# Performance work log

Measured on AMD Instinct MI355X. Metric: run time of the kernel, lower is better.

Reference implementation:

```python
import jax, jax.numpy as jnp
import numpy as np

N = 8            # n_qubits
N_LAYERS_CRZ = 1

_H = jnp.array([[1.0, 1.0], [1.0, -1.0]], dtype=jnp.complex64) / np.sqrt(2).astype(np.float32)
_X2 = jnp.array([[0.0, 1.0], [1.0, 0.0]], dtype=jnp.complex64)
_I2 = jnp.eye(2, dtype=jnp.complex64)


def _apply_1q(state, U, q):
    # shared (2,2) gate on wire q; state: (B, 2,...,2)
    moved = jnp.moveaxis(state, 1 + q, -1)
    out = jnp.einsum('ij,...j->...i', U, moved)
    return jnp.moveaxis(out, -1, 1 + q)


def _apply_1q_batched(state, U, q):
    # per-sample (B,2,2) gate on wire q
    moved = jnp.moveaxis(state, 1 + q, -1)
    out = jnp.einsum('bij,b...j->b...i', U, moved)
    return jnp.moveaxis(out, -1, 1 + q)


def _apply_diag_batched(state, d, q):
    # per-sample diagonal (B,2) phases on wire q
    shape = (d.shape[0],) + (1,) * q + (2,) + (1,) * (N - 1 - q)
    return state * d.reshape(shape)


def _apply_ctrl_diag(state, ph, c, t):
    # controlled diagonal: apply phases ph (2,) on target t when control c == 1
    moved = jnp.moveaxis(state, (1 + c, 1 + t), (-2, -1))
    d = jnp.stack([jnp.ones(2, state.dtype), ph])  # (bc, bt)
    moved = moved * d
    return jnp.moveaxis(moved, (-2, -1), (1 + c, 1 + t))


def _apply_ctrl(state, U, c, t):
    # controlled (2,2) gate, control c, target t
    moved = jnp.moveaxis(state, (1 + c, 1 + t), (-2, -1))
    s0 = moved[..., 0, :]
    s1 = jnp.einsum('ij,...j->...i', U, moved[..., 1, :])
    out = jnp.stack([s0, s1], axis=-2)
    return jnp.moveaxis(out, (-2, -1), (1 + c, 1 + t))


def _circuit(X, weights):
    B = X.shape[0]
    state = jnp.zeros((B,) + (2,) * N, jnp.complex64)
    state = state.at[(slice(None),) + (0,) * N].set(1.0)

    # encoding: H, RZ(x[2q]), RY(x[2q+1]) on each wire q (2q+1 < 16 always)
    for q in range(N):
        state = _apply_1q(state, _H, q)
        th_z = X[:, 2 * q]
        d = jnp.stack([jnp.exp(-0.5j * th_z), jnp.exp(0.5j * th_z)], axis=-1)  # (B,2)
        state = _apply_diag_batched(state, d, q)
        half = 0.5 * X[:, 2 * q + 1]
        c, s = jnp.cos(half), jnp.sin(half)
        Ury = jnp.stack([jnp.stack([c, -s], -1), jnp.stack([s, c], -1)], -2)  # (B,2,2) real
        state = _apply_1q_batched(state, Ury, q)

    # CRZ ring
    for l in range(N_LAYERS_CRZ):
        for i in range(N):
            th = weights[l, i]
            ph = jnp.stack([jnp.exp(-0.5j * th), jnp.exp(0.5j * th)])
            state = _apply_ctrl_diag(state, ph, i, (i + 1) % N)

    # all-to-all CRX
    for i in range(N):
        for j in range(N):
            if j == i:
                continue
            half = 0.5 * weights[N_LAYERS_CRZ + i, j]
            Urx = jnp.cos(half) * _I2 + (-1j * jnp.sin(half)) * _X2
            state = _apply_ctrl(state, Urx, i, j)

    probs = jnp.real(state * jnp.conj(state)).reshape(B, 2 ** N)
    q_idx = jnp.arange(N)
    bits = (jnp.arange(2 ** N)[None, :] >> (N - 1 - q_idx)[:, None]) & 1  # (N, 2^N)
    signs = (1.0 - 2.0 * bits).astype(probs.dtype)
    return probs @ signs.T  # (B, N) <Z_q> expectations


def setup_inputs() -> dict:
    key = jax.random.key(0)
    k1, k2 = jax.random.split(key)
    X = jax.random.normal(k1, (16384, 2 * N), dtype=jnp.float32)
    weights = jax.random.normal(k2, (N_LAYERS_CRZ + N, (N_LAYERS_CRZ + N) * N), dtype=jnp.float32)
    return {"X": X, "weights": weights}


def reference(X, weights):
    return _circuit(X, weights)
```

## Files before the change

kernel.cpp:

```cpp
#include <hip/hip_runtime.h>


static __device__ __forceinline__ float rlane(float v, int src) {
    return __int_as_float(__builtin_amdgcn_readlane(__float_as_int(v), src));
}
template <int CTRL>
static __device__ __forceinline__ float dppf(float x) {
    return __int_as_float(__builtin_amdgcn_update_dpp(0, __float_as_int(x), CTRL, 0xF, 0xF, true));
}
static __device__ __forceinline__ float xor1f(float x) { return dppf<0xB1>(x); }
static __device__ __forceinline__ float xor2f(float x) { return dppf<0x4E>(x); }
static __device__ __forceinline__ float xor4f(float x) { return dppf<0x1B>(dppf<0x141>(x)); }
static __device__ __forceinline__ float xor8f(float x) { return dppf<0x128>(x); }

__global__ __launch_bounds__(256, 4) void qsim_kernel(const float* __restrict__ X,
                                                      const float* __restrict__ W,
                                                      float* __restrict__ out,
                                                      int B) {
    const int lane = threadIdx.x & 63;
    const int g = lane >> 4;
    const int s = lane & 15;
    const int b = (blockIdx.x * 4 + (threadIdx.x >> 6)) * 4 + g;
    const bool active = (b < B);
    const int bc = active ? b : (B - 1);

    float gcv = 1.0f, gsv = 0.0f;
    if (lane < 56) {
        const int i = lane / 7;
        const int jj = lane - 7 * i;
        const int j = jj + (jj >= i ? 1 : 0);
        const float h = 0.5f * W[(1 + i) * 72 + j];
        __sincosf(h, &gsv, &gcv);
    }

    float u0r, u0i, u1r, u1i;
    {
        const int q = s & 7;
        float2 xq = ((const float2*)X)[bc * 8 + q];
        float cz, sz, cy, sy;
        __sincosf(0.5f * xq.x, &sz, &cz);
        __sincosf(0.5f * xq.y, &sy, &cy);
        u0r = (cy - sy) * cz;  u0i = -(cy + sy) * sz;
        u1r = (cy + sy) * cz;  u1i = (cy - sy) * sz;
    }

    float Pr = 1.0f, Pi = 0.0f;
#pragma unroll
    for (int q = 0; q < 4; ++q) {
        const int src = (g << 4) + q;
        const float a0r = __shfl(u0r, src, 64), a0i = __shfl(u0i, src, 64);
        const float a1r = __shfl(u1r, src, 64), a1i = __shfl(u1i, src, 64);
        const int bit = (s >> (3 - q)) & 1;
        const float vr = bit ? a1r : a0r;
        const float vi = bit ? a1i : a0i;
        const float nr = Pr * vr - Pi * vi;
        const float ni = Pr * vi + Pi * vr;
        Pr = nr; Pi = ni;
    }
    float w0r[4], w0i[4], w1r[4], w1i[4];
#pragma unroll
    for (int q = 4; q < 8; ++q) {
        const int src = (g << 4) + q;
        w0r[q - 4] = __shfl(u0r, src, 64);  w0i[q - 4] = __shfl(u0i, src, 64);
        w1r[q - 4] = __shfl(u1r, src, 64);  w1i[q - 4] = __shfl(u1i, src, 64);
    }
    float ar[16], ai[16];
    {
        float t1r[2], t1i[2];
        t1r[0] = w0r[0]; t1i[0] = w0i[0];
        t1r[1] = w1r[0]; t1i[1] = w1i[0];
        float t2r[4], t2i[4];
#pragma unroll
        for (int h = 0; h < 2; ++h) {
            t2r[h * 2 + 0] = t1r[h] * w0r[1] - t1i[h] * w0i[1];
            t2i[h * 2 + 0] = t1r[h] * w0i[1] + t1i[h] * w0r[1];
            t2r[h * 2 + 1] = t1r[h] * w1r[1] - t1i[h] * w1i[1];
            t2i[h * 2 + 1] = t1r[h] * w1i[1] + t1i[h] * w1r[1];
        }
        float t3r[8], t3i[8];
#pragma unroll
        for (int h = 0; h < 4; ++h) {
            t3r[h * 2 + 0] = t2r[h] * w0r[2] - t2i[h] * w0i[2];
            t3i[h * 2 + 0] = t2r[h] * w0i[2] + t2i[h] * w0r[2];
            t3r[h * 2 + 1] = t2r[h] * w1r[2] - t2i[h] * w1i[2];
            t3i[h * 2 + 1] = t2r[h] * w1i[2] + t2i[h] * w1r[2];
        }
#pragma unroll
        for (int h = 0; h < 8; ++h) {
            const float m0r = t3r[h] * w0r[3] - t3i[h] * w0i[3];
            const float m0i = t3r[h] * w0i[3] + t3i[h] * w0r[3];
            const float m1r = t3r[h] * w1r[3] - t3i[h] * w1i[3];
            const float m1i = t3r[h] * w1i[3] + t3i[h] * w1r[3];
            ar[h * 2 + 0] = Pr * m0r - Pi * m0i;
            ai[h * 2 + 0] = Pr * m0i + Pi * m0r;
            ar[h * 2 + 1] = Pr * m1r - Pi * m1i;
            ai[h * 2 + 1] = Pr * m1i + Pi * m1r;
        }
    }

    {
        const float w0 = W[0], w1 = W[1], w2 = W[2], w3 = W[3];
        const float w4 = W[4], w5 = W[5], w6 = W[6], w7 = W[7];
        const int b7 = (s >> 3) & 1, b6 = (s >> 2) & 1, b5 = (s >> 1) & 1, b4 = s & 1;
        float phiS = 0.0f;
        phiS += b7 ? (b6 ? w0 : -w0) : 0.0f;
        phiS += b6 ? (b5 ? w1 : -w1) : 0.0f;
        phiS += b5 ? (b4 ? w2 : -w2) : 0.0f;
        const float term3 = b4 ? w3 : 0.0f;
        const float term7 = b7 ? w7 : -w7;
#pragma unroll
        for (int r = 0; r < 16; ++r) {
            const int b3 = (r >> 3) & 1, b2 = (r >> 2) & 1, b1 = (r >> 1) & 1, b0 = r & 1;
            float phi = phiS + (b3 ? term3 : -term3);
            if (b3) phi += b2 ? w4 : -w4;
            if (b2) phi += b1 ? w5 : -w5;
            if (b1) phi += b0 ? w6 : -w6;
            if (b0) phi += term7;
            float sp, cp;
            __sincosf(0.5f * phi, &sp, &cp);
            const float nr = ar[r] * cp - ai[r] * sp;
            const float ni = ar[r] * sp + ai[r] * cp;
            ar[r] = nr; ai[r] = ni;
        }
    }

#pragma unroll
    for (int i = 0; i < 8; ++i) {
#pragma unroll
        for (int j = 0; j < 8; ++j) {
            if (j == i) continue;
            const int gi = i * 7 + (j < i ? j : j - 1);
            const float c = rlane(gcv, gi);
            const float sn = rlane(gsv, gi);
            const int pc = 7 - i, pt = 7 - j;
            float ce, se;
            if (pc >= 4) {
                const int ctrl = (s >> (pc - 4)) & 1;
                ce = ctrl ? c : 1.0f;
                se = ctrl ? sn : 0.0f;
            } else {
                ce = c; se = sn;
            }
            if (pt >= 4) {
                const int ms = 1 << (pt - 4);
#pragma unroll
                for (int r = 0; r < 16; ++r) {
                    if (pc < 4 && !((r >> pc) & 1)) continue;
                    float prr, pii;
                    if (ms == 1)      { prr = xor1f(ar[r]); pii = xor1f(ai[r]); }
                    else if (ms == 2) { prr = xor2f(ar[r]); pii = xor2f(ai[r]); }
                    else if (ms == 4) { prr = xor4f(ar[r]); pii = xor4f(ai[r]); }
                    else              { prr = xor8f(ar[r]); pii = xor8f(ai[r]); }
                    ar[r] = ce * ar[r] + se * pii;
                    ai[r] = ce * ai[r] - se * prr;
                }
            } else {
                const int mt = 1 << pt;
#pragma unroll
                for (int r = 0; r < 16; ++r) {
                    if (r & mt) continue;
                    if (pc < 4 && !((r >> pc) & 1)) continue;
                    const int rp = r | mt;
                    const float tr = ar[r],  ti = ai[r];
                    const float ur = ar[rp], ui = ai[rp];
                    ar[r]  = ce * tr + se * ui;
                    ai[r]  = ce * ti - se * ur;
                    ar[rp] = ce * ur + se * ti;
                    ai[rp] = ce * ui - se * tr;
                }
            }
        }
    }

    float p[16];
#pragma unroll
    for (int r = 0; r < 16; ++r) p[r] = ar[r] * ar[r] + ai[r] * ai[r];
    float s8[8], E7 = 0.0f;
#pragma unroll
    for (int k = 0; k < 8; ++k) { s8[k] = p[2 * k] + p[2 * k + 1]; E7 += p[2 * k] - p[2 * k + 1]; }
    float s4[4], E6 = 0.0f;
#pragma unroll
    for (int k = 0; k < 4; ++k) { s4[k] = s8[2 * k] + s8[2 * k + 1]; E6 += s8[2 * k] - s8[2 * k + 1]; }
    float s2a[2], E5 = 0.0f;
#pragma unroll
    for (int k = 0; k < 2; ++k) { s2a[k] = s4[2 * k] + s4[2 * k + 1]; E5 += s4[2 * k] - s4[2 * k + 1]; }
    float A  = s2a[0] + s2a[1];
    float E4 = s2a[0] - s2a[1];
    float D0, D1, D2, D3;
    { const float t = xor1f(A); D0 = A - t; A += t;
      E4 += xor1f(E4); E5 += xor1f(E5); E6 += xor1f(E6); E7 += xor1f(E7); }
    { const float t = xor2f(A); D1 = A - t; A += t;
      D0 += xor2f(D0);
      E4 += xor2f(E4); E5 += xor2f(E5); E6 += xor2f(E6); E7 += xor2f(E7); }
    { const float t = xor4f(A); D2 = A - t; A += t;
      D0 += xor4f(D0); D1 += xor4f(D1);
      E4 += xor4f(E4); E5 += xor4f(E5); E6 += xor4f(E6); E7 += xor4f(E7); }
    { const float t = xor8f(A); D3 = A - t;
      D0 += xor8f(D0); D1 += xor8f(D1); D2 += xor8f(D2);
      E4 += xor8f(E4); E5 += xor8f(E5); E6 += xor8f(E6); E7 += xor8f(E7); }

    if (s == 0 && active) {
        const float sc = 1.0f / 256.0f;
        float* o = out + b * 8;
        o[0] = D3 * sc;
        o[1] = D2 * sc;
        o[2] = D1 * sc;
        o[3] = D0 * sc;
        o[4] = E4 * sc;
        o[5] = E5 * sc;
        o[6] = E6 * sc;
        o[7] = E7 * sc;
    }
}

extern "C" void kernel_launch(void* const* d_in, const int* in_sizes, int n_in,
                              void* d_out, int out_size, void* d_ws, size_t ws_size,
                              hipStream_t stream) {
    const float* X = (const float*)d_in[0];
    const float* W = (const float*)d_in[1];
    float* out = (float*)d_out;
    const int B = in_sizes[0] / 16;
    const int blocks = (B + 15) / 16;
    qsim_kernel<<<blocks, 256, 0, stream>>>(X, W, out, B);
}
```

Baseline: 78.18 us.

## Swap register/lane qubit mapping midway so controls stay in registers

Remaps the state so that the first four control qubits live in the register index rather than the lane index. Their CRX gates then only touch the half of the registers where the control bit is set, instead of using per-lane select on the control. A 4-stage DPP transpose then swaps register and lane bits so the remaining four controls are also register-resident. This drops the wasted work on inactive-control amplitudes, at the cost of the transpose shuffles. The encoding and CRZ phase code are re-indexed to match the new layout.

Result: no change. 78.06 us (-0.1%).

```diff
diff --git a/kernel.cpp b/kernel.cpp
--- a/kernel.cpp
+++ b/kernel.cpp
@@ -12,6 +12,12 @@
 static __device__ __forceinline__ float xor2f(float x) { return dppf<0x4E>(x); }
 static __device__ __forceinline__ float xor4f(float x) { return dppf<0x1B>(dppf<0x141>(x)); }
 static __device__ __forceinline__ float xor8f(float x) { return dppf<0x128>(x); }
+static __device__ __forceinline__ float xorMf(float x, int m) {
+    if (m == 1) return xor1f(x);
+    if (m == 2) return xor2f(x);
+    if (m == 4) return xor4f(x);
+    return xor8f(x);
+}
 
 __global__ __launch_bounds__(256, 4) void qsim_kernel(const float* __restrict__ X,
                                                       const float* __restrict__ W,
@@ -46,11 +52,11 @@
 
     float Pr = 1.0f, Pi = 0.0f;
 #pragma unroll
-    for (int q = 0; q < 4; ++q) {
+    for (int q = 4; q < 8; ++q) {
         const int src = (g << 4) + q;
         const float a0r = __shfl(u0r, src, 64), a0i = __shfl(u0i, src, 64);
         const float a1r = __shfl(u1r, src, 64), a1i = __shfl(u1i, src, 64);
-        const int bit = (s >> (3 - q)) & 1;
+        const int bit = (s >> (7 - q)) & 1;
         const float vr = bit ? a1r : a0r;
         const float vi = bit ? a1i : a0i;
         const float nr = Pr * vr - Pi * vi;
@@ -59,10 +65,10 @@
     }
     float w0r[4], w0i[4], w1r[4], w1i[4];
 #pragma unroll
-    for (int q = 4; q < 8; ++q) {
-        const int src = (g << 4) + q;
-        w0r[q - 4] = __shfl(u0r, src, 64);  w0i[q - 4] = __shfl(u0i, src, 64);
-        w1r[q - 4] = __shfl(u1r, src, 64);  w1i[q - 4] = __shfl(u1i, src, 64);
+    for (int k = 0; k < 4; ++k) {
+        const int src = (g << 4) + k;
+        w0r[k] = __shfl(u0r, src, 64);  w0i[k] = __shfl(u0i, src, 64);
+        w1r[k] = __shfl(u1r, src, 64);  w1i[k] = __shfl(u1i, src, 64);
     }
     float ar[16], ai[16];
     {
@@ -101,21 +107,21 @@
     {
         const float w0 = W[0], w1 = W[1], w2 = W[2], w3 = W[3];
         const float w4 = W[4], w5 = W[5], w6 = W[6], w7 = W[7];
-        const int b7 = (s >> 3) & 1, b6 = (s >> 2) & 1, b5 = (s >> 1) & 1, b4 = s & 1;
+        const int s3 = (s >> 3) & 1, s2 = (s >> 2) & 1, s1 = (s >> 1) & 1, s0 = s & 1;
         float phiS = 0.0f;
-        phiS += b7 ? (b6 ? w0 : -w0) : 0.0f;
-        phiS += b6 ? (b5 ? w1 : -w1) : 0.0f;
-        phiS += b5 ? (b4 ? w2 : -w2) : 0.0f;
-        const float term3 = b4 ? w3 : 0.0f;
-        const float term7 = b7 ? w7 : -w7;
+        phiS += s3 ? (s2 ? w4 : -w4) : 0.0f;
+        phiS += s2 ? (s1 ? w5 : -w5) : 0.0f;
+        phiS += s1 ? (s0 ? w6 : -w6) : 0.0f;
+        const float termA = s3 ? w3 : -w3;
+        const float termB = s0 ? w7 : 0.0f;
 #pragma unroll
         for (int r = 0; r < 16; ++r) {
             const int b3 = (r >> 3) & 1, b2 = (r >> 2) & 1, b1 = (r >> 1) & 1, b0 = r & 1;
-            float phi = phiS + (b3 ? term3 : -term3);
-            if (b3) phi += b2 ? w4 : -w4;
-            if (b2) phi += b1 ? w5 : -w5;
-            if (b1) phi += b0 ? w6 : -w6;
-            if (b0) phi += term7;
+            float phi = phiS + (b3 ? termB : -termB);
+            if (b3) phi += b2 ? w0 : -w0;
+            if (b2) phi += b1 ? w1 : -w1;
+            if (b1) phi += b0 ? w2 : -w2;
+            if (b0) phi += termA;
             float sp, cp;
             __sincosf(0.5f * phi, &sp, &cp);
             const float nr = ar[r] * cp - ai[r] * sp;
@@ -125,48 +131,100 @@
     }
 
 #pragma unroll
-    for (int i = 0; i < 8; ++i) {
+    for (int i = 0; i < 4; ++i) {
+        float cg[8], sg[8];
 #pragma unroll
         for (int j = 0; j < 8; ++j) {
             if (j == i) continue;
             const int gi = i * 7 + (j < i ? j : j - 1);
-            const float c = rlane(gcv, gi);
-            const float sn = rlane(gsv, gi);
-            const int pc = 7 - i, pt = 7 - j;
-            float ce, se;
-            if (pc >= 4) {
-                const int ctrl = (s >> (pc - 4)) & 1;
-                ce = ctrl ? c : 1.0f;
-                se = ctrl ? sn : 0.0f;
-            } else {
-                ce = c; se = sn;
-            }
-            if (pt >= 4) {
-                const int ms = 1 << (pt - 4);
-#pragma unroll
-                for (int r = 0; r < 16; ++r) {
-                    if (pc < 4 && !((r >> pc) & 1)) continue;
-                    float prr, pii;
-                    if (ms == 1)      { prr = xor1f(ar[r]); pii = xor1f(ai[r]); }
-                    else if (ms == 2) { prr = xor2f(ar[r]); pii = xor2f(ai[r]); }
-                    else if (ms == 4) { prr = xor4f(ar[r]); pii = xor4f(ai[r]); }
-                    else              { prr = xor8f(ar[r]); pii = xor8f(ai[r]); }
-                    ar[r] = ce * ar[r] + se * pii;
-                    ai[r] = ce * ai[r] - se * prr;
-                }
-            } else {
-                const int mt = 1 << pt;
-#pragma unroll
-                for (int r = 0; r < 16; ++r) {
+            cg[j] = rlane(gcv, gi);
+            sg[j] = rlane(gsv, gi);
+        }
+        const int rc = 3 - i;
+#pragma unroll
+        for (int j = 0; j < 8; ++j) {
+            if (j == i) continue;
+            if (j < 4) {
+                const int mt = 1 << (3 - j);
+#pragma unroll
+                for (int r = 0; r < 16; ++r) {
+                    if (!((r >> rc) & 1)) continue;
                     if (r & mt) continue;
-                    if (pc < 4 && !((r >> pc) & 1)) continue;
                     const int rp = r | mt;
                     const float tr = ar[r],  ti = ai[r];
                     const float ur = ar[rp], ui = ai[rp];
-                    ar[r]  = ce * tr + se * ui;
-                    ai[r]  = ce * ti - se * ur;
-                    ar[rp] = ce * ur + se * ti;
-                    ai[rp] = ce * ui - se * tr;
+                    ar[r]  = cg[j] * tr + sg[j] * ui;
+                    ai[r]  = cg[j] * ti - sg[j] * ur;
+                    ar[rp] = cg[j] * ur + sg[j] * ti;
+                    ai[rp] = cg[j] * ui - sg[j] * tr;
+                }
+            } else {
+                const int ms = 1 << (7 - j);
+#pragma unroll
+                for (int r = 0; r < 16; ++r) {
+                    if (!((r >> rc) & 1)) continue;
+                    const float prr = xorMf(ar[r], ms);
+                    const float pii = xorMf(ai[r], ms);
+                    ar[r] = cg[j] * ar[r] + sg[j] * pii;
+                    ai[r] = cg[j] * ai[r] - sg[j] * prr;
+                }
+            }
+        }
+    }
+
+#pragma unroll
+    for (int k = 1; k <= 8; k <<= 1) {
+        const bool sk = (s & k) != 0;
+#pragma unroll
+        for (int r = 0; r < 16; ++r) {
+            if (r & k) continue;
+            const int rp = r | k;
+            const float tpr = xorMf(ar[rp], k), tpi = xorMf(ai[rp], k);
+            const float trr = xorMf(ar[r],  k), tri = xorMf(ai[r],  k);
+            ar[r]  = sk ? tpr : ar[r];
+            ai[r]  = sk ? tpi : ai[r];
+            ar[rp] = sk ? ar[rp] : trr;
+            ai[rp] = sk ? ai[rp] : tri;
+        }
+    }
+
+#pragma unroll
+    for (int i = 4; i < 8; ++i) {
+        float cg[8], sg[8];
+#pragma unroll
+        for (int j = 0; j < 8; ++j) {
+            if (j == i) continue;
+            const int gi = i * 7 + (j < i ? j : j - 1);
+            cg[j] = rlane(gcv, gi);
+            sg[j] = rlane(gsv, gi);
+        }
+        const int rc = 7 - i;
+#pragma unroll
+        for (int j = 0; j < 8; ++j) {
+            if (j == i) continue;
+            if (j < 4) {
+                const int ms = 1 << (3 - j);
+#pragma unroll
+                for (int r = 0; r < 16; ++r) {
+                    if (!((r >> rc) & 1)) continue;
+                    const float prr = xorMf(ar[r], ms);
+                    const float pii = xorMf(ai[r], ms);
+                    ar[r] = cg[j] * ar[r] + sg[j] * pii;
+                    ai[r] = cg[j] * ai[r] - sg[j] * prr;
+                }
+            } else {
+                const int mt = 1 << (7 - j);
+#pragma unroll
+                for (int r = 0; r < 16; ++r) {
+                    if (!((r >> rc) & 1)) continue;
+                    if (r & mt) continue;
+                    const int rp = r | mt;
+                    const float tr = ar[r],  ti = ai[r];
+                    const float ur = ar[rp], ui = ai[rp];
+                    ar[r]  = cg[j] * tr + sg[j] * ui;
+                    ai[r]  = cg[j] * ti - sg[j] * ur;
+                    ar[rp] = cg[j] * ur + sg[j] * ti;
+                    ai[rp] = cg[j] * ui - sg[j] * tr;
                 }
             }
         }
```
